# Kernel optimization log

Hardware: AMD Instinct MI355X
Metric: run time of the kernel (lower is better)

The kernel has to match this reference:

```python
import jax, jax.numpy as jnp
import numpy as np

N_NODES = 50000
N_EDGES = 800000
IN_DIM = 128
HID = 64
N_GRAPHS = 256


def setup_inputs() -> dict:
    key = jax.random.key(0)
    ks = jax.random.split(key, 10)
    s = lambda d: 1.0 / np.sqrt(d)
    return {
        'x': jax.random.normal(ks[0], (N_NODES, IN_DIM), jnp.float32),
        'edge_index': jax.random.randint(ks[1], (2, N_EDGES), 0, N_NODES, jnp.int64),
        'batch': jnp.sort(jax.random.randint(ks[2], (N_NODES,), 0, N_GRAPHS, jnp.int64)),
        'Wp': jax.random.normal(ks[3], (IN_DIM, HID), jnp.float32) * s(IN_DIM),
        'bp': jnp.zeros((HID,), jnp.float32),
        'W1_0': jax.random.normal(ks[4], (HID, HID), jnp.float32) * s(HID),
        'b1_0': jnp.zeros((HID,), jnp.float32),
        'W2_0': jax.random.normal(ks[5], (HID, HID), jnp.float32) * s(HID),
        'b2_0': jnp.zeros((HID,), jnp.float32),
        'W1_1': jax.random.normal(ks[6], (HID, HID), jnp.float32) * s(HID),
        'b1_1': jnp.zeros((HID,), jnp.float32),
        'W2_1': jax.random.normal(ks[7], (HID, HID), jnp.float32) * s(HID),
        'b2_1': jnp.zeros((HID,), jnp.float32),
    }


def _gin_layer(h, src, dst, W1, b1, W2, b2):
    # scatter-add aggregation: sum_{j in N(i)} h_j  (messages flow src -> dst)
    agg = jax.ops.segment_sum(h[src], dst, num_segments=N_NODES)
    z = h + agg  # eps = 0 (GINConv default)
    z = jax.nn.relu(z @ W1 + b1)
    z = z @ W2 + b2
    return jax.nn.relu(z)  # outer activation from SharedGINEncoder


def reference(x, edge_index, batch, Wp, bp, W1_0, b1_0, W2_0, b2_0, W1_1, b1_1, W2_1, b2_1):
    src, dst = edge_index[0], edge_index[1]
    h = jax.nn.relu(x @ Wp + bp)  # [N, HID]
    h = _gin_layer(h, src, dst, W1_0, b1_0, W2_0, b2_0)
    h = _gin_layer(h, src, dst, W1_1, b1_1, W2_1, b2_1)
    # global_mean_pool over graph ids
    sums = jax.ops.segment_sum(h, batch, num_segments=N_GRAPHS)  # [G, HID]
    counts = jax.ops.segment_sum(jnp.ones((h.shape[0],), h.dtype), batch, num_segments=N_GRAPHS)
    return sums / jnp.maximum(counts, 1.0)[:, None]
```

## Files before the change

kernel.cpp:

```cpp
#include <hip/hip_runtime.h>

#define N_NODES 50000
#define N_EDGES 800000
#define IN_DIM 128
#define HID 64
#define N_GRAPHS 256

#define E_PER_BLK 4000
#define F_BLOCKS (N_EDGES / E_PER_BLK)
#define NBKT ((N_NODES + 255) / 256)
#define CNT_N (NBKT * F_BLOCKS)
#define SCB ((CNT_N + 255) / 256)
#define NTILES (N_NODES / 4)
#define MTILES (N_NODES / 16)


__device__ __forceinline__ float bf2f(unsigned short v) {
  return __uint_as_float(((unsigned int)v) << 16);
}
__device__ __forceinline__ unsigned short f2bf(float f) {
  unsigned int u = __float_as_uint(f);
  return (unsigned short)((u + 0x7fffu + ((u >> 16) & 1u)) >> 16);
}

typedef __attribute__((ext_vector_type(8))) short bf16x8;
typedef __attribute__((ext_vector_type(4))) float f32x4;

__global__ __launch_bounds__(256) void part_hist_kernel(const int* __restrict__ dst,
                                                        int* __restrict__ cnt) {
  __shared__ int h[NBKT];
  const int t = threadIdx.x;
  for (int k = t; k < NBKT; k += 256) h[k] = 0;
  __syncthreads();
  const int base = blockIdx.x * E_PER_BLK;
  for (int i = t; i < E_PER_BLK; i += 256) atomicAdd(&h[dst[base + i] >> 8], 1);
  __syncthreads();
  for (int k = t; k < NBKT; k += 256) cnt[k * F_BLOCKS + blockIdx.x] = h[k];
}

__global__ __launch_bounds__(256) void scan1g_kernel(const int* __restrict__ in,
                                                     int* __restrict__ ex,
                                                     int* __restrict__ bsum, int n) {
  __shared__ int s[256];
  const int t = threadIdx.x;
  const int i = blockIdx.x * 256 + t;
  int v = (i < n) ? in[i] : 0;
  s[t] = v;
  __syncthreads();
#pragma unroll
  for (int ofs = 1; ofs < 256; ofs <<= 1) {
    int u = (t >= ofs) ? s[t - ofs] : 0;
    __syncthreads();
    s[t] += u;
    __syncthreads();
  }
  if (i < n) ex[i] = s[t] - v;
  if (t == 255) bsum[blockIdx.x] = s[255];
}

__global__ __launch_bounds__(256) void scan2g_kernel(const int* __restrict__ bsum,
                                                     int* __restrict__ bpref, int nb) {
  __shared__ int s[256];
  const int t = threadIdx.x;
  int v = (t < nb) ? bsum[t] : 0;
  s[t] = v;
  __syncthreads();
#pragma unroll
  for (int ofs = 1; ofs < 256; ofs <<= 1) {
    int u = (t >= ofs) ? s[t - ofs] : 0;
    __syncthreads();
    s[t] += u;
    __syncthreads();
  }
  if (t < nb) bpref[t] = s[t] - v;
}

__global__ __launch_bounds__(256) void part_scatter_kernel(const int* __restrict__ src,
                                                           const int* __restrict__ dst,
                                                           const int* __restrict__ cex,
                                                           const int* __restrict__ bpref,
                                                           int* __restrict__ psrc,
                                                           int* __restrict__ pdst) {
  __shared__ int cur[NBKT];
  const int t = threadIdx.x;
  for (int k = t; k < NBKT; k += 256) {
    const int i = k * F_BLOCKS + blockIdx.x;
    cur[k] = cex[i] + bpref[i >> 8];
  }
  __syncthreads();
  const int base = blockIdx.x * E_PER_BLK;
  for (int i = t; i < E_PER_BLK; i += 256) {
    int d = dst[base + i], s = src[base + i];
    int p = atomicAdd(&cur[d >> 8], 1);
    pdst[p] = d;
    psrc[p] = s;
  }
}

__global__ __launch_bounds__(256) void bucket_sort_kernel(const int* __restrict__ psrc,
                                                          const int* __restrict__ pdst,
                                                          const int* __restrict__ cex,
                                                          const int* __restrict__ bpref,
                                                          int* __restrict__ csr,
                                                          int* __restrict__ off) {
  const int k = blockIdx.x;
  const int t = threadIdx.x;
  const int i0 = k * F_BLOCKS;
  const int b0 = cex[i0] + bpref[i0 >> 8];
  int b1 = N_EDGES;
  if (k != NBKT - 1) {
    const int i1 = (k + 1) * F_BLOCKS;
    b1 = cex[i1] + bpref[i1 >> 8];
  }
  __shared__ int cnt[256];
  __shared__ int s[256];
  __shared__ int cur[256];
  cnt[t] = 0;
  __syncthreads();
  for (int i = b0 + t; i < b1; i += 256) atomicAdd(&cnt[pdst[i] & 255], 1);
  __syncthreads();
  int v = cnt[t];
  s[t] = v;
  __syncthreads();
#pragma unroll
  for (int ofs = 1; ofs < 256; ofs <<= 1) {
    int u = (t >= ofs) ? s[t - ofs] : 0;
    __syncthreads();
    s[t] += u;
    __syncthreads();
  }
  const int node = (k << 8) + t;
  const int start = b0 + s[t] - v;
  cur[t] = start;
  if (node < N_NODES) off[node] = start;
  if (k == NBKT - 1 && t == 0) off[N_NODES] = N_EDGES;
  __syncthreads();
  for (int i = b0 + t; i < b1; i += 256) {
    int d = pdst[i];
    int p = atomicAdd(&cur[d & 255], 1);
    csr[p] = psrc[i];
  }
}

__global__ __launch_bounds__(256) void proj_kernel(
    const float* __restrict__ x, const float* __restrict__ Wp,
    const float* __restrict__ bp, unsigned short* __restrict__ h) {
  __shared__ __align__(16) float sX[2][2][4][64];
  __shared__ __align__(16) float sPart[2][2][4][64];
  const int wave = threadIdx.x >> 6, lane = threadIdx.x & 63;
  const int pair = wave >> 1, khalf = wave & 1;
  float w[64];
#pragma unroll
  for (int k = 0; k < 64; ++k) w[k] = Wp[(khalf * 64 + k) * HID + lane];
  const float bias = bp[lane];
  const int pv = blockIdx.x * 2 + pair;
  const int np = gridDim.x * 2;
  const int iters = (NTILES - blockIdx.x * 2 + np - 1) / np;
  for (int it = 0; it < iters; ++it) {
    const int tile = pv + it * np;
    const bool act = (tile < NTILES);
    const int n0 = tile * 4;
    const int buf = it & 1;
    if (act) {
#pragma unroll
      for (int t = 0; t < 4; ++t)
        sX[pair][khalf][t][lane] = x[(n0 + t) * IN_DIM + khalf * 64 + lane];
    }
    float p[4];
#pragma unroll
    for (int t = 0; t < 4; ++t) {
      float a0 = khalf ? 0.f : bias, a1 = 0.f, a2 = 0.f, a3 = 0.f;
#pragma unroll
      for (int k = 0; k < 64; k += 4) {
        float4 v = *(const float4*)&sX[pair][khalf][t][k];
        a0 = fmaf(v.x, w[k + 0], a0);
        a1 = fmaf(v.y, w[k + 1], a1);
        a2 = fmaf(v.z, w[k + 2], a2);
        a3 = fmaf(v.w, w[k + 3], a3);
      }
      p[t] = (a0 + a1) + (a2 + a3);
    }
    if (act && khalf) {
#pragma unroll
      for (int t = 0; t < 4; ++t) sPart[pair][buf][t][lane] = p[t];
    }
    __syncthreads();
    if (act && !khalf) {
#pragma unroll
      for (int t = 0; t < 4; ++t)
        h[(n0 + t) * HID + lane] = f2bf(fmaxf(p[t] + sPart[pair][buf][t][lane], 0.0f));
    }
  }
}

__global__ __launch_bounds__(256) void gin_fused_mfma_kernel(
    const unsigned short* __restrict__ h_in, const int* __restrict__ off,
    const int* __restrict__ csr, const float* __restrict__ W1,
    const float* __restrict__ b1, const float* __restrict__ W2,
    const float* __restrict__ b2, unsigned short* __restrict__ h_out) {
  __shared__ __align__(16) unsigned short sW1[4096];
  __shared__ __align__(16) unsigned short sW2[4096];
  __shared__ __align__(16) unsigned short sT[4][16][72];
  const int t = threadIdx.x;
  for (int i = t; i < 4096; i += 256) {
    const int k = i >> 6, j = i & 63;
    const int pos = (((j >> 4) * 2 + (k >> 5)) * 64 + ((k >> 3) & 3) * 16 + (j & 15)) * 8 + (k & 7);
    sW1[pos] = f2bf(W1[i]);
    sW2[pos] = f2bf(W2[i]);
  }
  __syncthreads();
  const int wave = t >> 6, lane = t & 63;
  const int row = lane & 15;
  const int kgrp = lane >> 4;
  float bias1[4], bias2[4];
#pragma unroll
  for (int nc = 0; nc < 4; ++nc) {
    bias1[nc] = b1[nc * 16 + row];
    bias2[nc] = b2[nc * 16 + row];
  }
  const uint4* __restrict__ hv = (const uint4*)h_in;
  const int tile = blockIdx.x * 4 + wave;
  if (tile < MTILES) {
    const int n0 = tile * 16;
    const int n = n0 + row;
    const int o0 = off[n];
    const int deg = off[n + 1] - o0;
    int dm = deg;
#pragma unroll
    for (int m = 1; m <= 8; m <<= 1) {
      int o = __shfl_xor(dm, m);
      dm = (o > dm) ? o : dm;
    }
    float ac0[8], ac1[8];
    {
      uint4 ua = hv[n * 8 + kgrp];
      uint4 ub = hv[n * 8 + 4 + kgrp];
      const unsigned int* pa = (const unsigned int*)&ua;
      const unsigned int* pb = (const unsigned int*)&ub;
#pragma unroll
      for (int e = 0; e < 4; ++e) {
        ac0[2 * e] = bf2f((unsigned short)(pa[e] & 0xffff));
        ac0[2 * e + 1] = bf2f((unsigned short)(pa[e] >> 16));
        ac1[2 * e] = bf2f((unsigned short)(pb[e] & 0xffff));
        ac1[2 * e + 1] = bf2f((unsigned short)(pb[e] >> 16));
      }
    }
    for (int j = 0; j < dm; j += 4) {
#pragma unroll
      for (int u = 0; u < 4; ++u) {
        const int jj = j + u;
        const int pos = o0 + ((jj < deg) ? jj : 0);
        const int idx = csr[(pos < N_EDGES) ? pos : (N_EDGES - 1)];
        const float m = (jj < deg) ? 1.0f : 0.0f;
        uint4 ua = hv[idx * 8 + kgrp];
        uint4 ub = hv[idx * 8 + 4 + kgrp];
        const unsigned int* pa = (const unsigned int*)&ua;
        const unsigned int* pb = (const unsigned int*)&ub;
#pragma unroll
        for (int e = 0; e < 4; ++e) {
          ac0[2 * e] = fmaf(m, bf2f((unsigned short)(pa[e] & 0xffff)), ac0[2 * e]);
          ac0[2 * e + 1] = fmaf(m, bf2f((unsigned short)(pa[e] >> 16)), ac0[2 * e + 1]);
          ac1[2 * e] = fmaf(m, bf2f((unsigned short)(pb[e] & 0xffff)), ac1[2 * e]);
          ac1[2 * e + 1] = fmaf(m, bf2f((unsigned short)(pb[e] >> 16)), ac1[2 * e + 1]);
        }
      }
    }
    bf16x8 a1[2];
#pragma unroll
    for (int e = 0; e < 8; ++e) {
      a1[0][e] = (short)f2bf(ac0[e]);
      a1[1][e] = (short)f2bf(ac1[e]);
    }
    f32x4 acc;
#pragma unroll
    for (int nc = 0; nc < 4; ++nc) {
      acc = (f32x4){bias1[nc], bias1[nc], bias1[nc], bias1[nc]};
#pragma unroll
      for (int ks = 0; ks < 2; ++ks) {
        bf16x8 bf = *(const bf16x8*)&sW1[((nc * 2 + ks) * 64 + lane) * 8];
        acc = __builtin_amdgcn_mfma_f32_16x16x32_bf16(a1[ks], bf, acc, 0, 0, 0);
      }
#pragma unroll
      for (int r = 0; r < 4; ++r)
        sT[wave][kgrp * 4 + r][nc * 16 + row] = f2bf(fmaxf(acc[r], 0.0f));
    }
    bf16x8 a2[2];
    a2[0] = *(const bf16x8*)&sT[wave][row][kgrp * 8];
    a2[1] = *(const bf16x8*)&sT[wave][row][32 + kgrp * 8];
#pragma unroll
    for (int nc = 0; nc < 4; ++nc) {
      acc = (f32x4){bias2[nc], bias2[nc], bias2[nc], bias2[nc]};
#pragma unroll
      for (int ks = 0; ks < 2; ++ks) {
        bf16x8 bf = *(const bf16x8*)&sW2[((nc * 2 + ks) * 64 + lane) * 8];
        acc = __builtin_amdgcn_mfma_f32_16x16x32_bf16(a2[ks], bf, acc, 0, 0, 0);
      }
#pragma unroll
      for (int r = 0; r < 4; ++r)
        sT[wave][kgrp * 4 + r][nc * 16 + row] = f2bf(fmaxf(acc[r], 0.0f));
    }
#pragma unroll
    for (int p = 0; p < 2; ++p) {
      const int idx2 = p * 64 + lane;
      const int ri = idx2 >> 3, ch = idx2 & 7;
      uint4 v = *(const uint4*)&sT[wave][ri][ch * 8];
      *(uint4*)&h_out[(n0 + ri) * HID + ch * 8] = v;
    }
  }
}

__global__ __launch_bounds__(256) void pool_kernel(const unsigned short* __restrict__ h,
                                                   const int* __restrict__ batch,
                                                   float* __restrict__ out) {
  const int g = blockIdx.x;
  int lo = 0, hi = N_NODES;
  while (lo < hi) {
    int mid = (lo + hi) >> 1;
    if (batch[mid] < g) lo = mid + 1; else hi = mid;
  }
  const int s = lo;
  hi = N_NODES;
  while (lo < hi) {
    int mid = (lo + hi) >> 1;
    if (batch[mid] < g + 1) lo = mid + 1; else hi = mid;
  }
  const int e = lo;
  const int wave = threadIdx.x >> 6, lane = threadIdx.x & 63;
  float a0 = 0.f, a1 = 0.f, a2 = 0.f, a3 = 0.f;
  int n = s + wave;
  for (; n + 12 < e; n += 16) {
    a0 += bf2f(h[n * HID + lane]);
    a1 += bf2f(h[(n + 4) * HID + lane]);
    a2 += bf2f(h[(n + 8) * HID + lane]);
    a3 += bf2f(h[(n + 12) * HID + lane]);
  }
  for (; n < e; n += 4) a0 += bf2f(h[n * HID + lane]);
  __shared__ float red[4][HID];
  red[wave][lane] = ((a0 + a1) + (a2 + a3));
  __syncthreads();
  if (wave == 0) {
    float v = red[0][lane] + red[1][lane] + red[2][lane] + red[3][lane];
    float cnt = (float)(e - s);
    out[g * HID + lane] = v / fmaxf(cnt, 1.0f);
  }
}

extern "C" void kernel_launch(void* const* d_in, const int* in_sizes, int n_in,
                              void* d_out, int out_size, void* d_ws, size_t ws_size,
                              hipStream_t stream) {
  const float* x    = (const float*)d_in[0];
  const int*   edge = (const int*)d_in[1];
  const int*   batch= (const int*)d_in[2];
  const float* Wp   = (const float*)d_in[3];
  const float* bp   = (const float*)d_in[4];
  const float* W1_0 = (const float*)d_in[5];
  const float* b1_0 = (const float*)d_in[6];
  const float* W2_0 = (const float*)d_in[7];
  const float* b2_0 = (const float*)d_in[8];
  const float* W1_1 = (const float*)d_in[9];
  const float* b1_1 = (const float*)d_in[10];
  const float* W2_1 = (const float*)d_in[11];
  const float* b2_1 = (const float*)d_in[12];
  const int* src = edge;
  const int* dst = edge + N_EDGES;
  float* out = (float*)d_out;

  const size_t NB = (size_t)N_NODES * HID;
  unsigned short* hA = (unsigned short*)d_ws;
  unsigned short* hB = hA + NB;
  int* off     = (int*)(hB + NB);
  int* cnt     = off + N_NODES + 1;
  int* cex     = cnt + CNT_N;
  int* sbsum   = cex + CNT_N;
  int* sbpref  = sbsum + SCB;
  int* pdst    = sbpref + SCB;
  int* psrc    = pdst + N_EDGES;
  int* csr     = psrc + N_EDGES;

  dim3 b256(256);

  part_hist_kernel<<<F_BLOCKS, b256, 0, stream>>>(dst, cnt);
  scan1g_kernel<<<SCB, b256, 0, stream>>>(cnt, cex, sbsum, CNT_N);
  scan2g_kernel<<<1, b256, 0, stream>>>(sbsum, sbpref, SCB);
  part_scatter_kernel<<<F_BLOCKS, b256, 0, stream>>>(src, dst, cex, sbpref, psrc, pdst);
  bucket_sort_kernel<<<NBKT, b256, 0, stream>>>(psrc, pdst, cex, sbpref, csr, off);

  proj_kernel<<<2048, b256, 0, stream>>>(x, Wp, bp, hA);

  gin_fused_mfma_kernel<<<782, b256, 0, stream>>>(hA, off, csr, W1_0, b1_0, W2_0, b2_0, hB);
  gin_fused_mfma_kernel<<<782, b256, 0, stream>>>(hB, off, csr, W1_1, b1_1, W2_1, b2_1, hA);

  pool_kernel<<<N_GRAPHS, b256, 0, stream>>>(hA, batch, out);
}
```

Before: 140.8 us.

## Sort nodes by degree so each MFMA tile aggregates similar-degree neighbors

Builds a degree histogram during bucket sort, scans it, and scatters node ids into a degree-sorted permutation. The fused GIN kernel then processes 16-node tiles taken from this permutation, so lanes in a tile share a similar loop trip count (the max-degree shuffle) and divergence and idle lanes are reduced. The cost is three extra small kernels, an indirect perm load, and scattered, less coalesced output row writes and input row reads.

```diff
diff --git a/kernel.cpp b/kernel.cpp
--- a/kernel.cpp
+++ b/kernel.cpp
@@ -13,6 +13,8 @@
 #define SCB ((CNT_N + 255) / 256)
 #define NTILES (N_NODES / 4)
 #define MTILES (N_NODES / 16)
+#define DCNT_N (64 * NBKT)
+#define DSCB ((DCNT_N + 255) / 256)
 
 
 __device__ __forceinline__ float bf2f(unsigned short v) {
@@ -102,7 +104,8 @@
                                                           const int* __restrict__ cex,
                                                           const int* __restrict__ bpref,
                                                           int* __restrict__ csr,
-                                                          int* __restrict__ off) {
+                                                          int* __restrict__ off,
+                                                          int* __restrict__ dcnt) {
   const int k = blockIdx.x;
   const int t = threadIdx.x;
   const int i0 = k * F_BLOCKS;
@@ -115,7 +118,9 @@
   __shared__ int cnt[256];
   __shared__ int s[256];
   __shared__ int cur[256];
+  __shared__ int dhist[64];
   cnt[t] = 0;
+  if (t < 64) dhist[t] = 0;
   __syncthreads();
   for (int i = b0 + t; i < b1; i += 256) atomicAdd(&cnt[pdst[i] & 255], 1);
   __syncthreads();
@@ -132,13 +137,37 @@
   const int node = (k << 8) + t;
   const int start = b0 + s[t] - v;
   cur[t] = start;
-  if (node < N_NODES) off[node] = start;
+  if (node < N_NODES) {
+    off[node] = start;
+    atomicAdd(&dhist[(v < 63) ? v : 63], 1);
+  }
   if (k == NBKT - 1 && t == 0) off[N_NODES] = N_EDGES;
   __syncthreads();
+  if (t < 64) dcnt[t * NBKT + k] = dhist[t];
   for (int i = b0 + t; i < b1; i += 256) {
     int d = pdst[i];
     int p = atomicAdd(&cur[d & 255], 1);
     csr[p] = psrc[i];
+  }
+}
+
+__global__ __launch_bounds__(256) void perm_scatter_kernel(const int* __restrict__ off,
+                                                           const int* __restrict__ dex,
+                                                           const int* __restrict__ dbpref,
+                                                           int* __restrict__ perm) {
+  __shared__ int cur[64];
+  const int k = blockIdx.x, t = threadIdx.x;
+  if (t < 64) {
+    const int i = t * NBKT + k;
+    cur[t] = dex[i] + dbpref[i >> 8];
+  }
+  __syncthreads();
+  const int node = (k << 8) + t;
+  if (node < N_NODES) {
+    int d = off[node + 1] - off[node];
+    d = (d < 63) ? d : 63;
+    int pos = atomicAdd(&cur[d], 1);
+    perm[pos] = node;
   }
 }
 
@@ -195,9 +224,10 @@
 
 __global__ __launch_bounds__(256) void gin_fused_mfma_kernel(
     const unsigned short* __restrict__ h_in, const int* __restrict__ off,
-    const int* __restrict__ csr, const float* __restrict__ W1,
-    const float* __restrict__ b1, const float* __restrict__ W2,
-    const float* __restrict__ b2, unsigned short* __restrict__ h_out) {
+    const int* __restrict__ csr, const int* __restrict__ perm,
+    const float* __restrict__ W1, const float* __restrict__ b1,
+    const float* __restrict__ W2, const float* __restrict__ b2,
+    unsigned short* __restrict__ h_out) {
   __shared__ __align__(16) unsigned short sW1[4096];
   __shared__ __align__(16) unsigned short sW2[4096];
   __shared__ __align__(16) unsigned short sT[4][16][72];
@@ -221,8 +251,7 @@
   const uint4* __restrict__ hv = (const uint4*)h_in;
   const int tile = blockIdx.x * 4 + wave;
   if (tile < MTILES) {
-    const int n0 = tile * 16;
-    const int n = n0 + row;
+    const int n = perm[(tile << 4) + row];
     const int o0 = off[n];
     const int deg = off[n + 1] - o0;
     int dm = deg;
@@ -303,8 +332,9 @@
     for (int p = 0; p < 2; ++p) {
       const int idx2 = p * 64 + lane;
       const int ri = idx2 >> 3, ch = idx2 & 7;
+      const int nodeo = perm[(tile << 4) + ri];
       uint4 v = *(const uint4*)&sT[wave][ri][ch * 8];
-      *(uint4*)&h_out[(n0 + ri) * HID + ch * 8] = v;
+      *(uint4*)&h_out[nodeo * HID + ch * 8] = v;
     }
   }
 }
@@ -373,7 +403,12 @@
   int* cex     = cnt + CNT_N;
   int* sbsum   = cex + CNT_N;
   int* sbpref  = sbsum + SCB;
-  int* pdst    = sbpref + SCB;
+  int* dcnt    = sbpref + SCB;
+  int* dex     = dcnt + DCNT_N;
+  int* dbsum   = dex + DCNT_N;
+  int* dbpref  = dbsum + DSCB;
+  int* perm    = dbpref + DSCB;
+  int* pdst    = perm + N_NODES;
   int* psrc    = pdst + N_EDGES;
   int* csr     = psrc + N_EDGES;
 
@@ -383,12 +418,16 @@
   scan1g_kernel<<<SCB, b256, 0, stream>>>(cnt, cex, sbsum, CNT_N);
   scan2g_kernel<<<1, b256, 0, stream>>>(sbsum, sbpref, SCB);
   part_scatter_kernel<<<F_BLOCKS, b256, 0, stream>>>(src, dst, cex, sbpref, psrc, pdst);
-  bucket_sort_kernel<<<NBKT, b256, 0, stream>>>(psrc, pdst, cex, sbpref, csr, off);
+  bucket_sort_kernel<<<NBKT, b256, 0, stream>>>(psrc, pdst, cex, sbpref, csr, off, dcnt);
+
+  scan1g_kernel<<<DSCB, b256, 0, stream>>>(dcnt, dex, dbsum, DCNT_N);
+  scan2g_kernel<<<1, b256, 0, stream>>>(dbsum, dbpref, DSCB);
+  perm_scatter_kernel<<<NBKT, b256, 0, stream>>>(off, dex, dbpref, perm);
 
   proj_kernel<<<2048, b256, 0, stream>>>(x, Wp, bp, hA);
 
-  gin_fused_mfma_kernel<<<782, b256, 0, stream>>>(hA, off, csr, W1_0, b1_0, W2_0, b2_0, hB);
-  gin_fused_mfma_kernel<<<782, b256, 0, stream>>>(hB, off, csr, W1_1, b1_1, W2_1, b2_1, hA);
+  gin_fused_mfma_kernel<<<782, b256, 0, stream>>>(hA, off, csr, perm, W1_0, b1_0, W2_0, b2_0, hB);
+  gin_fused_mfma_kernel<<<782, b256, 0, stream>>>(hB, off, csr, perm, W1_1, b1_1, W2_1, b2_1, hA);
 
   pool_kernel<<<N_GRAPHS, b256, 0, stream>>>(hA, batch, out);
 }
```

Measured after the change: 133.2 us. -5.4%, faster.
